# Kernel tuning notes

Measured on AMD Instinct MI355X. Metric: run time of the kernel, lower is better.

## Reference

```python
import jax, jax.numpy as jnp
import numpy as np

N = 100000
E = 1600000
D = 64
ETA = 0.5
NEG_SLOPE = 0.01  # torch F.leaky_relu default


def setup_inputs() -> dict:
    key = jax.random.key(0)
    ks = jax.random.split(key, 6)
    h = jax.random.normal(ks[0], (N, D), dtype=jnp.float32)
    tax = jax.random.normal(ks[1], (N, D), dtype=jnp.float32)
    src = jax.random.randint(ks[2], (E,), 0, N, dtype=jnp.int32)
    dst = jax.random.randint(ks[3], (E,), 0, N, dtype=jnp.int32)
    # xavier_normal for Linear weights
    wh_w = jax.random.normal(ks[4], (1, 2 * D), dtype=jnp.float32) * np.sqrt(2.0 / (2 * D + 1))
    W_w = jax.random.normal(ks[5], (D, D), dtype=jnp.float32) * np.sqrt(2.0 / (D + D))
    W_b = jnp.zeros((D,), dtype=jnp.float32)
    return {"h": h, "tax": tax, "src": src, "dst": dst,
            "wh_w": wh_w, "W_w": W_w, "W_b": W_b}


def _edge_softmax(logits, dst):
    # logits: [E, 1]; softmax over edges grouped by destination node
    m = jax.ops.segment_max(logits, dst, num_segments=N)            # [N, 1]
    m = jnp.where(jnp.isfinite(m), m, 0.0)                          # nodes w/o in-edges
    e = jnp.exp(logits - m[dst])                                    # [E, 1]
    s = jax.ops.segment_sum(e, dst, num_segments=N)                 # [N, 1]
    return e / s[dst]


def reference(h, tax, src, dst, wh_w, W_w, W_b):
    hs, hd = h[src], h[dst]                                         # [E, D] gathers
    wf = jax.nn.leaky_relu(jnp.concatenate([hs, hd], axis=1) @ wh_w.T,
                           negative_slope=NEG_SLOPE)                # [E, 1]
    alpha_f = _edge_softmax(wf, dst)
    wt = jnp.sum(tax[src] * tax[dst], axis=1, keepdims=True)        # [E, 1]
    alpha_t = _edge_softmax(wt, dst)
    alpha = ETA * alpha_f + (1.0 - ETA) * alpha_t                   # [E, 1]
    z = jax.ops.segment_sum(hs * alpha, dst, num_segments=N)        # [N, D]
    return z @ W_w.T + W_b
```

## Files before the change

### kernel.cpp

```cpp
#include <hip/hip_runtime.h>

#define NEG_SLOPE 0.01f
#define ETA 0.5f
#define NEG_BIG -3.402823466e38f
#define LOG2E 1.4426950408889634f
#define PCHUNK 16384
#define CAP 1536
#define NBMAX 1568
#define GSTRIDE 16
#define ZPAD 36

typedef _Float16 half2v __attribute__((ext_vector_type(2)));
typedef _Float16 half8v __attribute__((ext_vector_type(8)));
typedef float f32x4v __attribute__((ext_vector_type(4)));

#if defined(__has_builtin)
#if __has_builtin(__builtin_amdgcn_fdot2)
#define HAVE_FDOT2 1
#endif
#if __has_builtin(__builtin_amdgcn_exp2f)
#define HAVE_EXP2 1
#endif
#if __has_builtin(__builtin_amdgcn_update_dpp)
#define HAVE_DPP 1
#endif
#if __has_builtin(__builtin_amdgcn_mfma_f32_16x16x32_f16)
#define HAVE_MFMA16 1
#endif
#endif

__device__ __forceinline__ float fdot2(half2v a, half2v b, float c) {
#ifdef HAVE_FDOT2
  return __builtin_amdgcn_fdot2(a, b, c, false);
#else
  return (float)a[0] * (float)b[0] + (float)a[1] * (float)b[1] + c;
#endif
}

__device__ __forceinline__ unsigned pack2(float x, float y) {
  half2v h = {( _Float16)x, (_Float16)y};
  return __builtin_bit_cast(unsigned, h);
}

__device__ __forceinline__ float fexp2(float x) {
#ifdef HAVE_EXP2
  return __builtin_amdgcn_exp2f(x);
#else
  return __expf(x * 0.6931471805599453f);
#endif
}

__device__ __forceinline__ void rowsum16x2(float& x, float& y) {
#ifdef HAVE_DPP
#define DPPADD(v, ctl)                                                        \
  v += __builtin_bit_cast(float, __builtin_amdgcn_update_dpp(                 \
         0, __builtin_bit_cast(int, v), ctl, 0xf, 0xf, true))
  DPPADD(x, 0x121); DPPADD(y, 0x121);
  DPPADD(x, 0x122); DPPADD(y, 0x122);
  DPPADD(x, 0x124); DPPADD(y, 0x124);
  DPPADD(x, 0x128); DPPADD(y, 0x128);
#undef DPPADD
#else
#pragma unroll
  for (int o = 1; o < 16; o <<= 1) {
    x += __shfl_xor(x, o);
    y += __shfl_xor(y, o);
  }
#endif
}

__device__ __forceinline__ void prep_body(const float* __restrict__ h,
                                          const float* __restrict__ tax,
                                          const float* __restrict__ whw,
                                          float* __restrict__ af, float* __restrict__ bf,
                                          uint4* __restrict__ rec, int n, int blk) {
  int gid = blk * 256 + (int)threadIdx.x;
  int node = gid >> 4, lane = gid & 15;
  if (node >= n) return;
  float4 x  = ((const float4*)(h + (size_t)node * 64))[lane];
  float4 tx = ((const float4*)(tax + (size_t)node * 64))[lane];
  float4 wa = ((const float4*)whw)[lane];
  float4 wb = ((const float4*)(whw + 64))[lane];
  uint4 r;
  r.x = pack2(tx.x, tx.y);
  r.y = pack2(tx.z, tx.w);
  r.z = pack2(x.x, x.y);
  r.w = pack2(x.z, x.w);
  rec[((size_t)node << 4) + lane] = r;
  float pa = x.x * wa.x + x.y * wa.y + x.z * wa.z + x.w * wa.w;
  float pb = x.x * wb.x + x.y * wb.y + x.z * wb.z + x.w * wb.w;
#pragma unroll
  for (int o = 8; o; o >>= 1) {
    pa += __shfl_xor(pa, o);
    pb += __shfl_xor(pb, o);
  }
  if (lane == 0) { af[node] = pa * LOG2E; bf[node] = pb * LOG2E; }
}

__device__ __forceinline__ void part_body(const int* __restrict__ src,
                                          const int* __restrict__ dst,
                                          int* __restrict__ gcur, int* __restrict__ pck,
                                          int ne, int nb, int blk) {
  __shared__ int s_hist[NBMAX];
  int t = threadIdx.x;
  int base = blk * PCHUNK;
  int cnt = ne - base; if (cnt > PCHUNK) cnt = PCHUNK;
  for (int j = t; j < nb; j += 256) s_hist[j] = 0;
  __syncthreads();
  int i = t * 4;
  for (; i + 3 < cnt; i += 1024) {
    int4 dd = *(const int4*)(dst + base + i);
    atomicAdd(&s_hist[dd.x >> 6], 1);
    atomicAdd(&s_hist[dd.y >> 6], 1);
    atomicAdd(&s_hist[dd.z >> 6], 1);
    atomicAdd(&s_hist[dd.w >> 6], 1);
  }
  for (; i < cnt; ++i) atomicAdd(&s_hist[dst[base + i] >> 6], 1);
  __syncthreads();
  for (int j = t; j < nb; j += 256) {
    int v = s_hist[j];
    if (v > 0) s_hist[j] = atomicAdd(&gcur[j * GSTRIDE], v);
  }
  __syncthreads();
  i = t * 4;
  for (; i + 3 < cnt; i += 1024) {
    int4 dd = *(const int4*)(dst + base + i);
    int4 ss = *(const int4*)(src + base + i);
    int r, g;
    r = dd.x >> 6; g = atomicAdd(&s_hist[r], 1);
    if (g < CAP) pck[(size_t)r * CAP + g] = (ss.x << 6) | (dd.x & 63);
    r = dd.y >> 6; g = atomicAdd(&s_hist[r], 1);
    if (g < CAP) pck[(size_t)r * CAP + g] = (ss.y << 6) | (dd.y & 63);
    r = dd.z >> 6; g = atomicAdd(&s_hist[r], 1);
    if (g < CAP) pck[(size_t)r * CAP + g] = (ss.z << 6) | (dd.z & 63);
    r = dd.w >> 6; g = atomicAdd(&s_hist[r], 1);
    if (g < CAP) pck[(size_t)r * CAP + g] = (ss.w << 6) | (dd.w & 63);
  }
  for (; i < cnt; ++i) {
    int d = dst[base + i];
    int r = d >> 6;
    int g = atomicAdd(&s_hist[r], 1);
    if (g < CAP) pck[(size_t)r * CAP + g] = (src[base + i] << 6) | (d & 63);
  }
}

__global__ void k_prep_part(const float* __restrict__ h, const float* __restrict__ tax,
                            const float* __restrict__ whw,
                            float* __restrict__ af, float* __restrict__ bf,
                            uint4* __restrict__ rec,
                            const int* __restrict__ src, const int* __restrict__ dst,
                            int* __restrict__ gcur, int* __restrict__ pck,
                            int n, int ne, int nb, int npart) {
  int b = (int)blockIdx.x;
  if (b < npart) part_body(src, dst, gcur, pck, ne, nb, b);
  else           prep_body(h, tax, whw, af, bf, rec, n, b - npart);
}

__launch_bounds__(256)
__global__ void k_fused(const uint4* __restrict__ rec,
                        const float* __restrict__ af, const float* __restrict__ bf,
                        const int* __restrict__ gcur, const int* __restrict__ pck,
                        const float* __restrict__ W, const float* __restrict__ bias,
                        float* __restrict__ out, int n) {
  __shared__ int s_hist[64];
  __shared__ int s_off[65];
  __shared__ int s_cur[64];
  __shared__ int s_srcs[CAP];
  __shared__ unsigned s_zu[64 * ZPAD];
  int b = (int)blockIdx.x;
  int t = (int)threadIdx.x;
  int cnt = gcur[b * GSTRIDE]; if (cnt > CAP) cnt = CAP;
  const int* pb = pck + (size_t)b * CAP;
  if (t < 64) s_hist[t] = 0;
  __syncthreads();
  for (int i = t; i < cnt; i += 256) atomicAdd(&s_hist[pb[i] & 63], 1);
  __syncthreads();
  if (t < 64) {
    int x = s_hist[t];
#pragma unroll
    for (int o = 1; o < 64; o <<= 1) {
      int y = __shfl_up(x, o);
      if (t >= o) x += y;
    }
    s_off[t + 1] = x;
    if (t == 0) s_off[0] = 0;
  }
  __syncthreads();
  if (t < 64) s_cur[t] = s_off[t];
  __syncthreads();
  for (int i = t; i < cnt; i += 256) {
    int p = pb[i];
    int r = atomicAdd(&s_cur[p & 63], 1);
    s_srcs[r] = p >> 6;
  }
  __syncthreads();
  int g = t >> 4, q = t & 15;
#pragma unroll
  for (int rnd = 0; rnd < 4; ++rnd) {
    int ld = g + (rnd << 4);
    int d = (b << 6) + ld;
    float4 zv = make_float4(0.f, 0.f, 0.f, 0.f);
    if (d < n) {
      uint2 rd = *(const uint2*)((const char*)rec + ((((size_t)d << 4) + q) << 4));
      half2v d01 = __builtin_bit_cast(half2v, rd.x);
      half2v d23 = __builtin_bit_cast(half2v, rd.y);
      float bfd = bf[d];
      int beg = s_off[ld], end = s_off[ld + 1];
      float sf = 0.f, st = 0.f, mt = NEG_BIG;
      float zf0 = 0.f, zf1 = 0.f, zf2 = 0.f, zf3 = 0.f;
      float zt0 = 0.f, zt1 = 0.f, zt2 = 0.f, zt3 = 0.f;
      int s0 = (beg     < end) ? s_srcs[beg]     : 0;
      int s1 = (beg + 1 < end) ? s_srcs[beg + 1] : 0;
      uint4 r0 = rec[((size_t)s0 << 4) + q];
      float a0 = af[s0];
      uint4 r1 = rec[((size_t)s1 << 4) + q];
      float a1 = af[s1];
      int s2 = (beg + 2 < end) ? s_srcs[beg + 2] : 0;
      int s3 = (beg + 3 < end) ? s_srcs[beg + 3] : 0;
      for (int i = beg; i < end; i += 2) {
        uint4 rn0 = rec[((size_t)s2 << 4) + q];
        float an0 = af[s2];
        uint4 rn1 = rec[((size_t)s3 << 4) + q];
        float an1 = af[s3];
        int s4 = (i + 4 < end) ? s_srcs[i + 4] : 0;
        int s5 = (i + 5 < end) ? s_srcs[i + 5] : 0;
        half2v t01a = __builtin_bit_cast(half2v, r0.x);
        half2v t23a = __builtin_bit_cast(half2v, r0.y);
        half2v h01a = __builtin_bit_cast(half2v, r0.z);
        half2v h23a = __builtin_bit_cast(half2v, r0.w);
        half2v t01b = __builtin_bit_cast(half2v, r1.x);
        half2v t23b = __builtin_bit_cast(half2v, r1.y);
        half2v h01b = __builtin_bit_cast(half2v, r1.z);
        half2v h23b = __builtin_bit_cast(half2v, r1.w);
        float p0 = fdot2(t23a, d23, fdot2(t01a, d01, 0.f)) * LOG2E;
        float p1 = fdot2(t23b, d23, fdot2(t01b, d01, 0.f)) * LOG2E;
        rowsum16x2(p0, p1);
        float wf0 = a0 + bfd;
        wf0 = (wf0 > 0.f) ? wf0 : NEG_SLOPE * wf0;
        float wf1 = a1 + bfd;
        wf1 = (wf1 > 0.f) ? wf1 : NEG_SLOPE * wf1;
        if (i + 1 >= end) { p1 = -1e30f; wf1 = -1e30f; }
        float ef0 = fexp2(wf0), ef1 = fexp2(wf1);
        sf += ef0 + ef1;
        zf0 = fmaf((float)h01b[0], ef1, fmaf((float)h01a[0], ef0, zf0));
        zf1 = fmaf((float)h01b[1], ef1, fmaf((float)h01a[1], ef0, zf1));
        zf2 = fmaf((float)h23b[0], ef1, fmaf((float)h23a[0], ef0, zf2));
        zf3 = fmaf((float)h23b[1], ef1, fmaf((float)h23a[1], ef0, zf3));
        float pm0 = p0 - mt;
        if (pm0 > 60.f) {
          float sc = fexp2(-pm0);
          st *= sc;
          zt0 *= sc; zt1 *= sc; zt2 *= sc; zt3 *= sc;
          mt = p0; pm0 = 0.f;
        }
        float et0 = fexp2(pm0);
        st += et0;
        zt0 = fmaf((float)h01a[0], et0, zt0);
        zt1 = fmaf((float)h01a[1], et0, zt1);
        zt2 = fmaf((float)h23a[0], et0, zt2);
        zt3 = fmaf((float)h23a[1], et0, zt3);
        float pm1 = p1 - mt;
        if (pm1 > 60.f) {
          float sc = fexp2(-pm1);
          st *= sc;
          zt0 *= sc; zt1 *= sc; zt2 *= sc; zt3 *= sc;
          mt = p1; pm1 = 0.f;
        }
        float et1 = fexp2(pm1);
        st += et1;
        zt0 = fmaf((float)h01b[0], et1, zt0);
        zt1 = fmaf((float)h01b[1], et1, zt1);
        zt2 = fmaf((float)h23b[0], et1, zt2);
        zt3 = fmaf((float)h23b[1], et1, zt3);
        r0 = rn0; a0 = an0; r1 = rn1; a1 = an1;
        s2 = s4;  s3 = s5;
      }
      if (end > beg) {
        float rf = ETA / sf, rt = (1.f - ETA) / st;
        zv.x = rf * zf0 + rt * zt0;
        zv.y = rf * zf1 + rt * zt1;
        zv.z = rf * zf2 + rt * zt2;
        zv.w = rf * zf3 + rt * zt3;
      }
    }
    s_zu[ld * ZPAD + 2 * q]     = pack2(zv.x, zv.y);
    s_zu[ld * ZPAD + 2 * q + 1] = pack2(zv.z, zv.w);
  }
  __syncthreads();
#ifdef HAVE_MFMA16
  {
    int l = t & 63, wv = t >> 6;
    int c16 = l & 15, seg = l >> 4;
    int rbase = wv << 4;
    const unsigned* za = s_zu + (size_t)(rbase + c16) * ZPAD;
    half8v a0 = __builtin_bit_cast(half8v, *(const uint4*)(za + seg * 4));
    half8v a1 = __builtin_bit_cast(half8v, *(const uint4*)(za + 16 + seg * 4));
#pragma unroll
    for (int jt = 0; jt < 4; ++jt) {
      int j = (jt << 4) + c16;
      const float* wr = W + (size_t)j * 64 + seg * 8;
      half8v bh0, bl0, bh1, bl1;
#pragma unroll
      for (int e = 0; e < 8; ++e) {
        float w0 = wr[e];
        _Float16 hi0 = (_Float16)w0;
        bh0[e] = hi0; bl0[e] = (_Float16)(w0 - (float)hi0);
        float w1 = wr[32 + e];
        _Float16 hi1 = (_Float16)w1;
        bh1[e] = hi1; bl1[e] = (_Float16)(w1 - (float)hi1);
      }
      float bj = bias[j];
      f32x4v acc = {bj, bj, bj, bj};
      acc = __builtin_amdgcn_mfma_f32_16x16x32_f16(a0, bh0, acc, 0, 0, 0);
      acc = __builtin_amdgcn_mfma_f32_16x16x32_f16(a1, bh1, acc, 0, 0, 0);
      acc = __builtin_amdgcn_mfma_f32_16x16x32_f16(a0, bl0, acc, 0, 0, 0);
      acc = __builtin_amdgcn_mfma_f32_16x16x32_f16(a1, bl1, acc, 0, 0, 0);
#pragma unroll
      for (int r = 0; r < 4; ++r) {
        int nrow = (b << 6) + rbase + (seg << 2) + r;
        if (nrow < n) out[(size_t)nrow * 64 + j] = acc[r];
      }
    }
  }
#else
  {
    int l = t & 63, wv = t >> 6;
    int c16 = l & 15, seg = l >> 4;
    int rbase = wv << 4;
#pragma unroll
    for (int jt = 0; jt < 4; ++jt) {
      int j = (jt << 4) + c16;
#pragma unroll
      for (int r = 0; r < 4; ++r) {
        int lrow = rbase + (seg << 2) + r;
        int nrow = (b << 6) + lrow;
        if (nrow >= n) continue;
        float acc = bias[j];
        const unsigned* zr = s_zu + (size_t)lrow * ZPAD;
        for (int k = 0; k < 32; ++k) {
          half2v hv = __builtin_bit_cast(half2v, zr[k]);
          acc += (float)hv[0] * W[(size_t)j * 64 + 2 * k]
               + (float)hv[1] * W[(size_t)j * 64 + 2 * k + 1];
        }
        out[(size_t)nrow * 64 + j] = acc;
      }
    }
  }
#endif
}

extern "C" void kernel_launch(void* const* d_in, const int* in_sizes, int n_in,
                              void* d_out, int out_size, void* d_ws, size_t ws_size,
                              hipStream_t stream) {
  const float* h   = (const float*)d_in[0];
  const float* tax = (const float*)d_in[1];
  const int*   src = (const int*)d_in[2];
  const int*   dst = (const int*)d_in[3];
  const float* whw = (const float*)d_in[4];
  const float* Ww  = (const float*)d_in[5];
  const float* Wb  = (const float*)d_in[6];
  float* out = (float*)d_out;
  int n  = in_sizes[0] / 64;
  int ne = in_sizes[2];
  int nb = (n + 63) >> 6;

  float* af   = (float*)d_ws;
  float* bf   = af + n;
  int*   gcur = (int*)(bf + n);
  int*   pck  = gcur + (size_t)NBMAX * GSTRIDE;
  size_t w = (size_t)(2 * n) + (size_t)NBMAX * GSTRIDE + (size_t)nb * CAP;
  w = (w + 3) & ~(size_t)3;
  uint4* rec = (uint4*)((int*)d_ws + w);

  int nprep = (n * 16 + 255) / 256;
  int npart = (ne + PCHUNK - 1) / PCHUNK;

  hipMemsetAsync(gcur, 0, (size_t)nb * GSTRIDE * sizeof(int), stream);
  k_prep_part<<<npart + nprep, 256, 0, stream>>>(h, tax, whw, af, bf, rec,
                                                 src, dst, gcur, pck, n, ne, nb, npart);
  k_fused<<<nb, 256, 0, stream>>>(rec, af, bf, gcur, pck, Ww, Wb, out, n);
}
```

Before: 219.3 us.

## Partition edges into coarse 256-node buckets with LDS-staged coalesced scatter

Edge partitioning now groups edges into 256-destination coarse buckets instead of 64-node blocks. Each partition block counting-sorts its chunk in shared memory before writing to global, so global writes become mostly contiguous runs. The fused kernel then has each of four 64-node blocks scan its shared coarse bucket and filter out its own edges. This trades scattered global writes and many global atomics for extra shared-memory work, and each fused block now reads four times as much bucket data.

```diff
diff --git a/kernel.cpp b/kernel.cpp
--- a/kernel.cpp
+++ b/kernel.cpp
@@ -4,9 +4,10 @@
 #define ETA 0.5f
 #define NEG_BIG -3.402823466e38f
 #define LOG2E 1.4426950408889634f
-#define PCHUNK 16384
-#define CAP 1536
-#define NBMAX 1568
+#define PCHUNK 4096
+#define CCAP 4608
+#define NCMAX 512
+#define TCAP 1536
 #define GSTRIDE 16
 #define ZPAD 36
 
@@ -100,47 +101,75 @@
 __device__ __forceinline__ void part_body(const int* __restrict__ src,
                                           const int* __restrict__ dst,
                                           int* __restrict__ gcur, int* __restrict__ pck,
-                                          int ne, int nb, int blk) {
-  __shared__ int s_hist[NBMAX];
+                                          int ne, int blk) {
+  __shared__ int s_h[NCMAX];
+  __shared__ int s_cur[NCMAX];
+  __shared__ int s_goff[NCMAX];
+  __shared__ int s_pair[256];
+  __shared__ int s_scr[PCHUNK];
+  __shared__ int s_gidx[PCHUNK];
   int t = threadIdx.x;
   int base = blk * PCHUNK;
   int cnt = ne - base; if (cnt > PCHUNK) cnt = PCHUNK;
-  for (int j = t; j < nb; j += 256) s_hist[j] = 0;
+  s_h[t] = 0; s_h[t + 256] = 0;
   __syncthreads();
   int i = t * 4;
   for (; i + 3 < cnt; i += 1024) {
     int4 dd = *(const int4*)(dst + base + i);
-    atomicAdd(&s_hist[dd.x >> 6], 1);
-    atomicAdd(&s_hist[dd.y >> 6], 1);
-    atomicAdd(&s_hist[dd.z >> 6], 1);
-    atomicAdd(&s_hist[dd.w >> 6], 1);
-  }
-  for (; i < cnt; ++i) atomicAdd(&s_hist[dst[base + i] >> 6], 1);
-  __syncthreads();
-  for (int j = t; j < nb; j += 256) {
-    int v = s_hist[j];
-    if (v > 0) s_hist[j] = atomicAdd(&gcur[j * GSTRIDE], v);
-  }
+    atomicAdd(&s_h[dd.x >> 8], 1);
+    atomicAdd(&s_h[dd.y >> 8], 1);
+    atomicAdd(&s_h[dd.z >> 8], 1);
+    atomicAdd(&s_h[dd.w >> 8], 1);
+  }
+  for (; i < cnt; ++i) atomicAdd(&s_h[dst[base + i] >> 8], 1);
+  __syncthreads();
+  int c0 = s_h[2 * t], c1 = s_h[2 * t + 1];
+  int v = c0 + c1;
+  s_pair[t] = v;
+  __syncthreads();
+  for (int s = 1; s < 256; s <<= 1) {
+    int a = (t >= s) ? s_pair[t - s] : 0;
+    __syncthreads();
+    s_pair[t] += a;
+    __syncthreads();
+  }
+  int pex = s_pair[t] - v;
+  int base0 = pex, base1 = pex + c0;
+  if (c0 > 0) {
+    int gb = atomicAdd(&gcur[(2 * t) * GSTRIDE], c0);
+    s_goff[2 * t] = (2 * t) * CCAP + gb - base0;
+  }
+  if (c1 > 0) {
+    int gb = atomicAdd(&gcur[(2 * t + 1) * GSTRIDE], c1);
+    s_goff[2 * t + 1] = (2 * t + 1) * CCAP + gb - base1;
+  }
+  s_cur[2 * t] = base0;
+  s_cur[2 * t + 1] = base1;
   __syncthreads();
   i = t * 4;
   for (; i + 3 < cnt; i += 1024) {
     int4 dd = *(const int4*)(dst + base + i);
     int4 ss = *(const int4*)(src + base + i);
-    int r, g;
-    r = dd.x >> 6; g = atomicAdd(&s_hist[r], 1);
-    if (g < CAP) pck[(size_t)r * CAP + g] = (ss.x << 6) | (dd.x & 63);
-    r = dd.y >> 6; g = atomicAdd(&s_hist[r], 1);
-    if (g < CAP) pck[(size_t)r * CAP + g] = (ss.y << 6) | (dd.y & 63);
-    r = dd.z >> 6; g = atomicAdd(&s_hist[r], 1);
-    if (g < CAP) pck[(size_t)r * CAP + g] = (ss.z << 6) | (dd.z & 63);
-    r = dd.w >> 6; g = atomicAdd(&s_hist[r], 1);
-    if (g < CAP) pck[(size_t)r * CAP + g] = (ss.w << 6) | (dd.w & 63);
+#define PSCAT(D, S)                                                           \
+    { int cb = (D) >> 8;                                                      \
+      int slot = atomicAdd(&s_cur[cb], 1);                                    \
+      int gl = slot + s_goff[cb];                                             \
+      s_scr[slot] = ((S) << 8) | ((D) & 255);                                 \
+      s_gidx[slot] = (gl < (cb + 1) * CCAP) ? gl : -1; }
+    PSCAT(dd.x, ss.x)
+    PSCAT(dd.y, ss.y)
+    PSCAT(dd.z, ss.z)
+    PSCAT(dd.w, ss.w)
   }
   for (; i < cnt; ++i) {
-    int d = dst[base + i];
-    int r = d >> 6;
-    int g = atomicAdd(&s_hist[r], 1);
-    if (g < CAP) pck[(size_t)r * CAP + g] = (src[base + i] << 6) | (d & 63);
+    int d = dst[base + i], s = src[base + i];
+    PSCAT(d, s)
+  }
+#undef PSCAT
+  __syncthreads();
+  for (int s = t; s < cnt; s += 256) {
+    int gi = s_gidx[s];
+    if (gi >= 0) pck[gi] = s_scr[s];
   }
 }
 
@@ -150,9 +179,9 @@
                             uint4* __restrict__ rec,
                             const int* __restrict__ src, const int* __restrict__ dst,
                             int* __restrict__ gcur, int* __restrict__ pck,
-                            int n, int ne, int nb, int npart) {
+                            int n, int ne, int npart) {
   int b = (int)blockIdx.x;
-  if (b < npart) part_body(src, dst, gcur, pck, ne, nb, b);
+  if (b < npart) part_body(src, dst, gcur, pck, ne, b);
   else           prep_body(h, tax, whw, af, bf, rec, n, b - npart);
 }
 
@@ -165,15 +194,33 @@
   __shared__ int s_hist[64];
   __shared__ int s_off[65];
   __shared__ int s_cur[64];
-  __shared__ int s_srcs[CAP];
+  __shared__ int s_cnt;
+  __shared__ int s_tmp[TCAP];
+  __shared__ int s_srcs[TCAP];
   __shared__ unsigned s_zu[64 * ZPAD];
   int b = (int)blockIdx.x;
   int t = (int)threadIdx.x;
-  int cnt = gcur[b * GSTRIDE]; if (cnt > CAP) cnt = CAP;
-  const int* pb = pck + (size_t)b * CAP;
+  int cb = b >> 2, sub = b & 3;
+  int cnt = gcur[cb * GSTRIDE]; if (cnt > CCAP) cnt = CCAP;
+  const int* pb = pck + (size_t)cb * CCAP;
   if (t < 64) s_hist[t] = 0;
-  __syncthreads();
-  for (int i = t; i < cnt; i += 256) atomicAdd(&s_hist[pb[i] & 63], 1);
+  if (t == 0) s_cnt = 0;
+  __syncthreads();
+  int i = t * 4;
+  for (; i + 3 < cnt; i += 1024) {
+    int4 e4 = *(const int4*)(pb + i);
+#define PFILT(E)                                                              \
+    if ((((E) >> 6) & 3) == sub) {                                            \
+      int k = atomicAdd(&s_cnt, 1);                                           \
+      if (k < TCAP) s_tmp[k] = (E);                                           \
+    }
+    PFILT(e4.x) PFILT(e4.y) PFILT(e4.z) PFILT(e4.w)
+  }
+  for (; i < cnt; ++i) { int e = pb[i]; PFILT(e) }
+#undef PFILT
+  __syncthreads();
+  int kc = s_cnt; if (kc > TCAP) kc = TCAP;
+  for (i = t; i < kc; i += 256) atomicAdd(&s_hist[s_tmp[i] & 63], 1);
   __syncthreads();
   if (t < 64) {
     int x = s_hist[t];
@@ -188,10 +235,10 @@
   __syncthreads();
   if (t < 64) s_cur[t] = s_off[t];
   __syncthreads();
-  for (int i = t; i < cnt; i += 256) {
-    int p = pb[i];
-    int r = atomicAdd(&s_cur[p & 63], 1);
-    s_srcs[r] = p >> 6;
+  for (i = t; i < kc; i += 256) {
+    int e = s_tmp[i];
+    int r = atomicAdd(&s_cur[e & 63], 1);
+    s_srcs[r] = e >> 8;
   }
   __syncthreads();
   int g = t >> 4, q = t & 15;
@@ -217,13 +264,13 @@
       float a1 = af[s1];
       int s2 = (beg + 2 < end) ? s_srcs[beg + 2] : 0;
       int s3 = (beg + 3 < end) ? s_srcs[beg + 3] : 0;
-      for (int i = beg; i < end; i += 2) {
+      for (int ii = beg; ii < end; ii += 2) {
         uint4 rn0 = rec[((size_t)s2 << 4) + q];
         float an0 = af[s2];
         uint4 rn1 = rec[((size_t)s3 << 4) + q];
         float an1 = af[s3];
-        int s4 = (i + 4 < end) ? s_srcs[i + 4] : 0;
-        int s5 = (i + 5 < end) ? s_srcs[i + 5] : 0;
+        int s4 = (ii + 4 < end) ? s_srcs[ii + 4] : 0;
+        int s5 = (ii + 5 < end) ? s_srcs[ii + 5] : 0;
         half2v t01a = __builtin_bit_cast(half2v, r0.x);
         half2v t23a = __builtin_bit_cast(half2v, r0.y);
         half2v h01a = __builtin_bit_cast(half2v, r0.z);
@@ -239,7 +286,7 @@
         wf0 = (wf0 > 0.f) ? wf0 : NEG_SLOPE * wf0;
         float wf1 = a1 + bfd;
         wf1 = (wf1 > 0.f) ? wf1 : NEG_SLOPE * wf1;
-        if (i + 1 >= end) { p1 = -1e30f; wf1 = -1e30f; }
+        if (ii + 1 >= end) { p1 = -1e30f; wf1 = -1e30f; }
         float ef0 = fexp2(wf0), ef1 = fexp2(wf1);
         sf += ef0 + ef1;
         zf0 = fmaf((float)h01b[0], ef1, fmaf((float)h01a[0], ef0, zf0));
@@ -367,16 +414,16 @@
   float* af   = (float*)d_ws;
   float* bf   = af + n;
   int*   gcur = (int*)(bf + n);
-  int*   pck  = gcur + (size_t)NBMAX * GSTRIDE;
-  size_t w = (size_t)(2 * n) + (size_t)NBMAX * GSTRIDE + (size_t)nb * CAP;
+  int*   pck  = gcur + (size_t)NCMAX * GSTRIDE;
+  size_t w = (size_t)(2 * n) + (size_t)NCMAX * GSTRIDE + (size_t)NCMAX * CCAP;
   w = (w + 3) & ~(size_t)3;
   uint4* rec = (uint4*)((int*)d_ws + w);
 
   int nprep = (n * 16 + 255) / 256;
   int npart = (ne + PCHUNK - 1) / PCHUNK;
 
-  hipMemsetAsync(gcur, 0, (size_t)nb * GSTRIDE * sizeof(int), stream);
+  hipMemsetAsync(gcur, 0, (size_t)NCMAX * GSTRIDE * sizeof(int), stream);
   k_prep_part<<<npart + nprep, 256, 0, stream>>>(h, tax, whw, af, bf, rec,
-                                                 src, dst, gcur, pck, n, ne, nb, npart);
+                                                 src, dst, gcur, pck, n, ne, npart);
   k_fused<<<nb, 256, 0, stream>>>(rec, af, bf, gcur, pck, Ww, Wb, out, n);
 }
```

Result: faster. 198.6 us (-9.4%).
